# Kernel optimization log

Measured on AMD Instinct MI355X. Metric: run time of the kernel, lower is better.

The kernel has to match this reference:

```python
import jax, jax.numpy as jnp
from jax import lax
import numpy as np

NUM_Q = 3000
EMB = 256
HID = 256
B, S = 32, 500


def _gru(x, w_ih, w_hh, b_ih, b_hh):
    """PyTorch-style single-layer GRU, batch_first. x: [B,S,E] -> [B,S,H]."""
    Bn = x.shape[0]
    H = w_hh.shape[1]
    # precompute input projections for all timesteps: [B,S,3H]
    x_proj = jnp.einsum('bse,ge->bsg', x, w_ih) + b_ih

    def step(h, xp):  # h: [B,H], xp: [B,3H]
        gh = h @ w_hh.T + b_hh
        xr, xz, xn = jnp.split(xp, 3, axis=-1)
        hr, hz, hn = jnp.split(gh, 3, axis=-1)
        r = jax.nn.sigmoid(xr + hr)
        z = jax.nn.sigmoid(xz + hz)
        n = jnp.tanh(xn + r * hn)
        h_new = (1.0 - z) * n + z * h
        return h_new, h_new

    h0 = jnp.zeros((Bn, H), x.dtype)
    _, out = lax.scan(step, h0, jnp.swapaxes(x_proj, 0, 1))  # [S,B,H]
    return jnp.swapaxes(out, 0, 1)


def setup_inputs() -> dict:
    key = jax.random.key(0)
    ks = jax.random.split(key, 16)
    sc = 0.05
    inp = {
        'x': jax.random.uniform(ks[0], (B, S, 2 * NUM_Q), dtype=jnp.float32),
        'ques_h': jax.random.normal(ks[1], (2 * NUM_Q, EMB), dtype=jnp.float32) * sc,
        'ques_d': jax.random.normal(ks[2], (2 * NUM_Q, EMB), dtype=jnp.float32) * sc,
        'gru1_wih': jax.random.normal(ks[3], (3 * HID, EMB), dtype=jnp.float32) * sc,
        'gru1_whh': jax.random.normal(ks[4], (3 * HID, HID), dtype=jnp.float32) * sc,
        'gru1_bih': jnp.zeros((3 * HID,), jnp.float32),
        'gru1_bhh': jnp.zeros((3 * HID,), jnp.float32),
        'gru2_wih': jax.random.normal(ks[5], (3 * HID, EMB), dtype=jnp.float32) * sc,
        'gru2_whh': jax.random.normal(ks[6], (3 * HID, HID), dtype=jnp.float32) * sc,
        'gru2_bih': jnp.zeros((3 * HID,), jnp.float32),
        'gru2_bhh': jnp.zeros((3 * HID,), jnp.float32),
        'fcc_w': jax.random.normal(ks[7], (NUM_Q, HID), dtype=jnp.float32) * sc,
        'fcc_b': jnp.zeros((NUM_Q,), jnp.float32),
        'fct_w': jax.random.normal(ks[8], (NUM_Q, HID), dtype=jnp.float32) * sc,
        'fct_b': jnp.zeros((NUM_Q,), jnp.float32),
        'fce_w': jax.random.normal(ks[9], (NUM_Q, 2 * HID), dtype=jnp.float32) * sc,
        'fce_b': jnp.zeros((NUM_Q,), jnp.float32),
    }
    return inp


def reference(x, ques_h, ques_d,
              gru1_wih, gru1_whh, gru1_bih, gru1_bhh,
              gru2_wih, gru2_whh, gru2_bih, gru2_bhh,
              fcc_w, fcc_b, fct_w, fct_b, fce_w, fce_b):
    # interaction embeddings via question tables
    x_h = jnp.einsum('bsq,qe->bse', x, ques_h)
    x_d = jnp.einsum('bsq,qe->bse', x, ques_d)
    # dual GRU encoders
    out_h = _gru(x_h, gru1_wih, gru1_whh, gru1_bih, gru1_bhh)  # [B,S,H]
    out_d = _gru(x_d, gru2_wih, gru2_whh, gru2_bih, gru2_bhh)  # [B,S,H]
    # per-branch logits
    logit_c = jnp.einsum('bsh,qh->bsq', out_h, fcc_w) + fcc_b
    logit_t = jnp.einsum('bsh,qh->bsq', out_d, fct_w) + fct_b
    # cross-attention fusion: matmul -> softmax -> bmm, plus inverse attention
    scores = jnp.einsum('bsh,bth->bst', out_h, out_d)  # [B,S,S]
    attn = jax.nn.softmax(scores, axis=2)
    fused_d = jnp.einsum('bst,bth->bsh', attn, out_d)
    fused_h = jnp.einsum('bst,bth->bsh', 1.0 - attn, out_h)
    ens = jnp.concatenate([fused_d, fused_h], axis=-1)  # [B,S,2H]
    ensemble_logit = jnp.einsum('bsk,qk->bsq', ens, fce_w) + fce_b
    return (logit_c, logit_t, ensemble_logit)
```

## Files before the change

### kernel.cpp

```cpp
#include <hip/hip_runtime.h>
#include <math.h>

#define BATCH 32
#define SEQ   500
#define NQ    3000
#define EMB   256
#define HID   256
#define ROWS  (BATCH * SEQ)
#define X_K   (2 * NQ)

typedef short short8 __attribute__((ext_vector_type(8)));
typedef float f32x4  __attribute__((ext_vector_type(4)));

__device__ __forceinline__ unsigned bf16_rne(float f) {
    unsigned u = __float_as_uint(f);
    return (u + 0x7fffu + ((u >> 16) & 1u)) >> 16;
}
__device__ __forceinline__ unsigned pack_bf16_rn(float a, float b) {
    return bf16_rne(a) | (bf16_rne(b) << 16);
}

__device__ __forceinline__ void stage_tile(unsigned char* lbase, int row, int cg, float4 v) {
    unsigned ux = __float_as_uint(v.x), uy = __float_as_uint(v.y);
    unsigned uz = __float_as_uint(v.z), uw = __float_as_uint(v.w);
    unsigned hx = ux & 0xffff0000u, hy = uy & 0xffff0000u;
    unsigned hz = uz & 0xffff0000u, hw = uw & 0xffff0000u;
    unsigned hi01 = (hx >> 16) | hy;
    unsigned hi23 = (hz >> 16) | hw;
    unsigned lo01 = pack_bf16_rn(v.x - __uint_as_float(hx), v.y - __uint_as_float(hy));
    unsigned lo23 = pack_bf16_rn(v.z - __uint_as_float(hz), v.w - __uint_as_float(hw));
    const int slot = cg ^ (row & 7);
    const int pf   = (row >> 3) & 1;
    uint4 w = pf ? make_uint4(lo01, lo23, hi01, hi23)
                 : make_uint4(hi01, hi23, lo01, lo23);
    *reinterpret_cast<uint4*>(lbase + row * 128 + (slot << 4)) = w;
}

__device__ __forceinline__ void read_frag(const unsigned char* lbase, int row, int c,
                                          short8& hi, short8& lo) {
    const int r7 = row & 7;
    const int pf = (row >> 3) & 1;
    const unsigned char* rbase = lbase + row * 128;
    const int s0 = (((c << 1) | 0) ^ r7) << 4;
    const int s1 = (((c << 1) | 1) ^ r7) << 4;
    const int oh = pf << 3;
    const int ol = (pf ^ 1) << 3;
    uint2 h0 = *reinterpret_cast<const uint2*>(rbase + s0 + oh);
    uint2 h1 = *reinterpret_cast<const uint2*>(rbase + s1 + oh);
    uint2 l0 = *reinterpret_cast<const uint2*>(rbase + s0 + ol);
    uint2 l1 = *reinterpret_cast<const uint2*>(rbase + s1 + ol);
    hi = __builtin_bit_cast(short8, make_uint4(h0.x, h0.y, h1.x, h1.y));
    lo = __builtin_bit_cast(short8, make_uint4(l0.x, l0.y, l1.x, l1.y));
}

template<bool HASBIAS>
__global__ __launch_bounds__(256, 2)
void gemm_mfma(const float* __restrict__ A, const float* __restrict__ B,
               const float* __restrict__ bias, float* __restrict__ C,
               int M, int N, int K, int ldc,
               long long sA, long long sB, long long sC)
{
    A += (long long)blockIdx.z * sA;
    B += (long long)blockIdx.z * sB;
    C += (long long)blockIdx.z * sC;

    __shared__ __align__(16) unsigned char lds[32768];
    unsigned char* Al_ = lds;
    unsigned char* Bl_ = lds + 16384;

    const int tid = threadIdx.x;
    const int m0 = blockIdx.y * 128;
    const int n0 = blockIdx.x * 128;

    const int srow = tid >> 3;
    const int scg  = tid & 7;

    const int wid = tid >> 6;
    const int wm  = wid >> 1;
    const int wn  = wid & 1;
    const int lane = tid & 63;
    const int fr  = lane & 15;
    const int fc  = lane >> 4;

    f32x4 acc[4][4];
    #pragma unroll
    for (int i = 0; i < 4; ++i)
        #pragma unroll
        for (int j = 0; j < 4; ++j)
            acc[i][j] = (f32x4){0.f, 0.f, 0.f, 0.f};

    const int ktiles = (K + 31) >> 5;
    for (int kt = 0; kt < ktiles; ++kt) {
        const int gk = (kt << 5) + scg * 4;
        #pragma unroll
        for (int rd = 0; rd < 4; ++rd) {
            const int row = rd * 32 + srow;
            {
                const int gm = m0 + row;
                float4 v = make_float4(0.f, 0.f, 0.f, 0.f);
                if (gm < M && gk < K)
                    v = *reinterpret_cast<const float4*>(A + (long long)gm * K + gk);
                stage_tile(Al_, row, scg, v);
            }
            {
                const int gn = n0 + row;
                float4 v = make_float4(0.f, 0.f, 0.f, 0.f);
                if (gn < N && gk < K)
                    v = *reinterpret_cast<const float4*>(B + (long long)gn * K + gk);
                stage_tile(Bl_, row, scg, v);
            }
        }
        __syncthreads();

        short8 ah[4], al[4], bh[4], bl[4];
        #pragma unroll
        for (int mi = 0; mi < 4; ++mi)
            read_frag(Al_, wm * 64 + mi * 16 + fr, fc, ah[mi], al[mi]);
        #pragma unroll
        for (int ni = 0; ni < 4; ++ni)
            read_frag(Bl_, wn * 64 + ni * 16 + fr, fc, bh[ni], bl[ni]);

        #pragma unroll
        for (int mi = 0; mi < 4; ++mi) {
            #pragma unroll
            for (int ni = 0; ni < 4; ++ni) {
                acc[mi][ni] = __builtin_amdgcn_mfma_f32_16x16x32_bf16(al[mi], bh[ni], acc[mi][ni], 0, 0, 0);
                acc[mi][ni] = __builtin_amdgcn_mfma_f32_16x16x32_bf16(ah[mi], bl[ni], acc[mi][ni], 0, 0, 0);
                acc[mi][ni] = __builtin_amdgcn_mfma_f32_16x16x32_bf16(ah[mi], bh[ni], acc[mi][ni], 0, 0, 0);
            }
        }
        __syncthreads();
    }

    #pragma unroll
    for (int ni = 0; ni < 4; ++ni) {
        const int col = n0 + wn * 64 + ni * 16 + fr;
        if (col >= N) continue;
        const float bv = HASBIAS ? bias[col] : 0.f;
        #pragma unroll
        for (int mi = 0; mi < 4; ++mi) {
            #pragma unroll
            for (int q = 0; q < 4; ++q) {
                const int rw = m0 + wm * 64 + mi * 16 + fc * 4 + q;
                if (rw < M) C[(long long)rw * ldc + col] = acc[mi][ni][q] + bv;
            }
        }
    }
}

__global__ __launch_bounds__(256)
void trans_kernel(const float* __restrict__ in, float* __restrict__ out,
                  int R, int C, long long sIn, long long sOut)
{
    in  += (long long)blockIdx.z * sIn;
    out += (long long)blockIdx.z * sOut;
    __shared__ float t[32][33];
    const int r0 = blockIdx.y * 32, c0 = blockIdx.x * 32;
    const int tx = threadIdx.x & 31, ty = threadIdx.x >> 5;
    #pragma unroll
    for (int i = 0; i < 32; i += 8) {
        const int r = r0 + ty + i, c = c0 + tx;
        t[ty + i][tx] = (r < R && c < C) ? in[(long long)r * C + c] : 0.f;
    }
    __syncthreads();
    #pragma unroll
    for (int i = 0; i < 32; i += 8) {
        const int r = r0 + tx, c = c0 + ty + i;
        if (c < C && r < R) out[(long long)c * R + r] = t[tx][ty + i];
    }
}

__global__ __launch_bounds__(256)
void gru_kernel(const float* __restrict__ xp1, const float* __restrict__ xp2,
                const float* __restrict__ wT1, const float* __restrict__ wT2,
                const float* __restrict__ bh1, const float* __restrict__ bh2,
                float* __restrict__ out1, float* __restrict__ out2)
{
    const int g = blockIdx.x >> 5;
    const int b = blockIdx.x & 31;
    const float* xp = (g ? xp2 : xp1) + (long long)b * SEQ * 768;
    const float* wT = g ? wT2 : wT1;
    const float* bh = g ? bh2 : bh1;
    float* out      = (g ? out2 : out1) + (long long)b * SEQ * HID;

    __shared__ float h[HID];
    const int j = threadIdx.x;
    h[j] = 0.f;
    const float br = bh[j], bz = bh[HID + j], bn = bh[2 * HID + j];
    __syncthreads();

    for (int t = 0; t < SEQ; ++t) {
        const float* xrow = xp + (long long)t * 768;
        float ar = br, az = bz, an = bn;
        #pragma unroll 8
        for (int k = 0; k < HID; ++k) {
            const float hk = h[k];
            const float* wrow = wT + k * 768;
            ar = fmaf(hk, wrow[j], ar);
            az = fmaf(hk, wrow[HID + j], az);
            an = fmaf(hk, wrow[2 * HID + j], an);
        }
        const float r = 1.f / (1.f + __expf(-(xrow[j] + ar)));
        const float z = 1.f / (1.f + __expf(-(xrow[HID + j] + az)));
        const float n = tanhf(xrow[2 * HID + j] + r * an);
        const float hnew = (1.f - z) * n + z * h[j];
        out[(long long)t * HID + j] = hnew;
        __syncthreads();
        h[j] = hnew;
        __syncthreads();
    }
}

__global__ __launch_bounds__(256)
void softmax_kernel(float* __restrict__ s)
{
    float* p = s + (long long)blockIdx.x * SEQ;
    const int tid = threadIdx.x;
    __shared__ float red[256];

    const float v0 = (tid < SEQ) ? p[tid] : -1e30f;
    const float v1 = (tid + 256 < SEQ) ? p[tid + 256] : -1e30f;
    red[tid] = fmaxf(v0, v1);
    __syncthreads();
    for (int o = 128; o > 0; o >>= 1) {
        if (tid < o) red[tid] = fmaxf(red[tid], red[tid + o]);
        __syncthreads();
    }
    const float m = red[0];
    __syncthreads();
    const float e0 = (tid < SEQ) ? __expf(v0 - m) : 0.f;
    const float e1 = (tid + 256 < SEQ) ? __expf(v1 - m) : 0.f;
    red[tid] = e0 + e1;
    __syncthreads();
    for (int o = 128; o > 0; o >>= 1) {
        if (tid < o) red[tid] += red[tid + o];
        __syncthreads();
    }
    const float inv = 1.f / red[0];
    if (tid < SEQ) p[tid] = e0 * inv;
    if (tid + 256 < SEQ) p[tid + 256] = e1 * inv;
}

__global__ __launch_bounds__(256)
void colsum_kernel(const float* __restrict__ x, float* __restrict__ out)
{
    const int b = blockIdx.x, hh = threadIdx.x;
    const float* p = x + (long long)b * SEQ * HID + hh;
    float s = 0.f;
    for (int t = 0; t < SEQ; ++t) s += p[t * HID];
    out[b * HID + hh] = s;
}

__global__ __launch_bounds__(256)
void combine_kernel(const float* __restrict__ tmp, const float* __restrict__ cs,
                    float* __restrict__ ens)
{
    const long long r = blockIdx.x;
    const int hh = threadIdx.x;
    const int b = (int)(r / SEQ);
    ens[r * 512 + 256 + hh] = cs[b * HID + hh] - tmp[r * HID + hh];
}

extern "C" void kernel_launch(void* const* d_in, const int* in_sizes, int n_in,
                              void* d_out, int out_size, void* d_ws, size_t ws_size,
                              hipStream_t stream)
{
    const float* x      = (const float*)d_in[0];
    const float* ques_h = (const float*)d_in[1];
    const float* ques_d = (const float*)d_in[2];
    const float* w1ih   = (const float*)d_in[3];
    const float* w1hh   = (const float*)d_in[4];
    const float* b1ih   = (const float*)d_in[5];
    const float* b1hh   = (const float*)d_in[6];
    const float* w2ih   = (const float*)d_in[7];
    const float* w2hh   = (const float*)d_in[8];
    const float* b2ih   = (const float*)d_in[9];
    const float* b2hh   = (const float*)d_in[10];
    const float* fcc_w  = (const float*)d_in[11];
    const float* fcc_b  = (const float*)d_in[12];
    const float* fct_w  = (const float*)d_in[13];
    const float* fct_b  = (const float*)d_in[14];
    const float* fce_w  = (const float*)d_in[15];
    const float* fce_b  = (const float*)d_in[16];

    float* ws = (float*)d_ws;
    float* xh    = ws;
    float* xd    = ws + 4096000LL;
    float* xp1   = ws + 8192000LL;
    float* xp2   = ws + 20480000LL;
    float* outh  = ws + 32768000LL;
    float* outd  = ws + 36864000LL;
    float* wT1   = ws + 40960000LL;
    float* wT2   = ws + 41156608LL;
    float* cs    = ws + 41353216LL;
    float* quesTh = xp1;
    float* quesTd = ws + 9728000LL;
    float* attn   = xp1;
    float* ens    = xp2;
    float* tmp    = ws + 28672000LL;
    float* outhT  = ws;
    float* outdT  = ws + 4096000LL;

    float* out_c = (float*)d_out;
    float* out_t = out_c + 48000000LL;
    float* out_e = out_c + 96000000LL;

    const dim3 blk(256);

    trans_kernel<<<dim3(8, 188, 1), blk, 0, stream>>>(ques_h, quesTh, X_K, EMB, 0, 0);
    trans_kernel<<<dim3(8, 188, 1), blk, 0, stream>>>(ques_d, quesTd, X_K, EMB, 0, 0);

    gemm_mfma<false><<<dim3(2, 125, 1), blk, 0, stream>>>(
        x, quesTh, nullptr, xh, ROWS, EMB, X_K, EMB, 0, 0, 0);
    gemm_mfma<false><<<dim3(2, 125, 1), blk, 0, stream>>>(
        x, quesTd, nullptr, xd, ROWS, EMB, X_K, EMB, 0, 0, 0);

    gemm_mfma<true><<<dim3(6, 125, 1), blk, 0, stream>>>(
        xh, w1ih, b1ih, xp1, ROWS, 768, EMB, 768, 0, 0, 0);
    gemm_mfma<true><<<dim3(6, 125, 1), blk, 0, stream>>>(
        xd, w2ih, b2ih, xp2, ROWS, 768, EMB, 768, 0, 0, 0);

    trans_kernel<<<dim3(8, 24, 1), blk, 0, stream>>>(w1hh, wT1, 768, 256, 0, 0);
    trans_kernel<<<dim3(8, 24, 1), blk, 0, stream>>>(w2hh, wT2, 768, 256, 0, 0);

    gru_kernel<<<64, blk, 0, stream>>>(xp1, xp2, wT1, wT2, b1hh, b2hh, outh, outd);

    gemm_mfma<true><<<dim3(24, 125, 1), blk, 0, stream>>>(
        outh, fcc_w, fcc_b, out_c, ROWS, NQ, HID, NQ, 0, 0, 0);
    gemm_mfma<true><<<dim3(24, 125, 1), blk, 0, stream>>>(
        outd, fct_w, fct_b, out_t, ROWS, NQ, HID, NQ, 0, 0, 0);

    trans_kernel<<<dim3(8, 16, 32), blk, 0, stream>>>(outh, outhT, SEQ, HID, 128000, 128000);
    trans_kernel<<<dim3(8, 16, 32), blk, 0, stream>>>(outd, outdT, SEQ, HID, 128000, 128000);

    gemm_mfma<false><<<dim3(4, 4, 32), blk, 0, stream>>>(
        outh, outd, nullptr, attn, SEQ, SEQ, HID, SEQ,
        (long long)SEQ * HID, (long long)SEQ * HID, (long long)SEQ * SEQ);

    softmax_kernel<<<ROWS, blk, 0, stream>>>(attn);

    colsum_kernel<<<32, blk, 0, stream>>>(outh, cs);

    gemm_mfma<false><<<dim3(2, 4, 32), blk, 0, stream>>>(
        attn, outdT, nullptr, ens, SEQ, HID, SEQ, 512,
        (long long)SEQ * SEQ, (long long)HID * SEQ, (long long)SEQ * 512);
    gemm_mfma<false><<<dim3(2, 4, 32), blk, 0, stream>>>(
        attn, outhT, nullptr, tmp, SEQ, HID, SEQ, HID,
        (long long)SEQ * SEQ, (long long)HID * SEQ, (long long)SEQ * HID);

    combine_kernel<<<ROWS, blk, 0, stream>>>(tmp, cs, ens);

    gemm_mfma<true><<<dim3(24, 125, 1), blk, 0, stream>>>(
        ens, fce_w, fce_b, out_e, ROWS, NQ, 512, NQ, 0, 0, 0);
}
```

Baseline: 7.202 ms.

## Split GRU recurrence K-dimension across threads and pack two batches per block

```diff
diff --git a/kernel.cpp b/kernel.cpp
--- a/kernel.cpp
+++ b/kernel.cpp
@@ -170,43 +170,65 @@
     }
 }
 
-__global__ __launch_bounds__(256)
+__global__ __launch_bounds__(1024)
 void gru_kernel(const float* __restrict__ xp1, const float* __restrict__ xp2,
                 const float* __restrict__ wT1, const float* __restrict__ wT2,
                 const float* __restrict__ bh1, const float* __restrict__ bh2,
                 float* __restrict__ out1, float* __restrict__ out2)
 {
-    const int g = blockIdx.x >> 5;
-    const int b = blockIdx.x & 31;
+    const int g   = blockIdx.x >> 4;
+    const int bp  = blockIdx.x & 15;
+    const int tid = threadIdx.x;
+    const int j   = tid & 255;
+    const int s   = (tid >> 8) & 1;
+    const int q   = tid >> 9;
+    const int b   = bp * 2 + s;
+
     const float* xp = (g ? xp2 : xp1) + (long long)b * SEQ * 768;
     const float* wT = g ? wT2 : wT1;
     const float* bh = g ? bh2 : bh1;
     float* out      = (g ? out2 : out1) + (long long)b * SEQ * HID;
 
-    __shared__ float h[HID];
-    const int j = threadIdx.x;
-    h[j] = 0.f;
-    const float br = bh[j], bz = bh[HID + j], bn = bh[2 * HID + j];
-    __syncthreads();
+    __shared__ float h[2][HID];
+    __shared__ float pacc[2][2][3][HID];
+
+    float br = 0.f, bz = 0.f, bn = 0.f;
+    if (tid < 512) {
+        h[s][j] = 0.f;
+        br = bh[j]; bz = bh[HID + j]; bn = bh[2 * HID + j];
+    }
+    __syncthreads();
+
+    const float* wbase = wT + (long long)q * 128 * 768;
+    const float* hrow  = &h[s][q * 128];
 
     for (int t = 0; t < SEQ; ++t) {
-        const float* xrow = xp + (long long)t * 768;
-        float ar = br, az = bz, an = bn;
+        float ar = 0.f, az = 0.f, an = 0.f;
         #pragma unroll 8
-        for (int k = 0; k < HID; ++k) {
-            const float hk = h[k];
-            const float* wrow = wT + k * 768;
+        for (int k = 0; k < 128; ++k) {
+            const float hk = hrow[k];
+            const float* wrow = wbase + k * 768;
             ar = fmaf(hk, wrow[j], ar);
             az = fmaf(hk, wrow[HID + j], az);
             an = fmaf(hk, wrow[2 * HID + j], an);
         }
-        const float r = 1.f / (1.f + __expf(-(xrow[j] + ar)));
-        const float z = 1.f / (1.f + __expf(-(xrow[HID + j] + az)));
-        const float n = tanhf(xrow[2 * HID + j] + r * an);
-        const float hnew = (1.f - z) * n + z * h[j];
-        out[(long long)t * HID + j] = hnew;
-        __syncthreads();
-        h[j] = hnew;
+        pacc[s][q][0][j] = ar;
+        pacc[s][q][1][j] = az;
+        pacc[s][q][2][j] = an;
+        __syncthreads();
+
+        if (tid < 512) {
+            const float* xrow = xp + (long long)t * 768;
+            const float gr = pacc[s][0][0][j] + pacc[s][1][0][j] + br;
+            const float gz = pacc[s][0][1][j] + pacc[s][1][1][j] + bz;
+            const float gn = pacc[s][0][2][j] + pacc[s][1][2][j] + bn;
+            const float r = 1.f / (1.f + __expf(-(xrow[j] + gr)));
+            const float z = 1.f / (1.f + __expf(-(xrow[HID + j] + gz)));
+            const float n = tanhf(xrow[2 * HID + j] + r * gn);
+            const float hnew = (1.f - z) * n + z * h[s][j];
+            out[(long long)t * HID + j] = hnew;
+            h[s][j] = hnew;
+        }
         __syncthreads();
     }
 }
@@ -323,7 +345,7 @@
     trans_kernel<<<dim3(8, 24, 1), blk, 0, stream>>>(w1hh, wT1, 768, 256, 0, 0);
     trans_kernel<<<dim3(8, 24, 1), blk, 0, stream>>>(w2hh, wT2, 768, 256, 0, 0);
 
-    gru_kernel<<<64, blk, 0, stream>>>(xp1, xp2, wT1, wT2, b1hh, b2hh, outh, outd);
+    gru_kernel<<<32, dim3(1024), 0, stream>>>(xp1, xp2, wT1, wT2, b1hh, b2hh, outh, outd);
 
     gemm_mfma<true><<<dim3(24, 125, 1), blk, 0, stream>>>(
         outh, fcc_w, fcc_b, out_c, ROWS, NQ, HID, NQ, 0, 0, 0);
```

Measured after the change: 9.166 ms. +27.3%, slower.

## Split GRU recurrence across four cooperating blocks with register-resident weights

Applied to the files above, without the earlier changes.

```diff
diff --git a/kernel.cpp b/kernel.cpp
--- a/kernel.cpp
+++ b/kernel.cpp
@@ -171,43 +171,124 @@
 }
 
 __global__ __launch_bounds__(256)
+void gru_init_kernel(float* __restrict__ h_g, unsigned* __restrict__ pflag,
+                     unsigned* __restrict__ hflag)
+{
+    const int i = blockIdx.x * 256 + threadIdx.x;
+    if (i < 64 * HID) h_g[i] = 0.f;
+    if (i < 64) { pflag[i] = 0u; hflag[i] = 0u; }
+}
+
+__global__ __launch_bounds__(256, 1)
 void gru_kernel(const float* __restrict__ xp1, const float* __restrict__ xp2,
                 const float* __restrict__ wT1, const float* __restrict__ wT2,
                 const float* __restrict__ bh1, const float* __restrict__ bh2,
-                float* __restrict__ out1, float* __restrict__ out2)
-{
-    const int g = blockIdx.x >> 5;
-    const int b = blockIdx.x & 31;
-    const float* xp = (g ? xp2 : xp1) + (long long)b * SEQ * 768;
+                float* __restrict__ out1, float* __restrict__ out2,
+                float* __restrict__ partials, float* __restrict__ h_g,
+                unsigned* __restrict__ pflag, unsigned* __restrict__ hflag)
+{
+    __shared__ float h_lds[HID];
+
+    const int bid = blockIdx.x;
+    const int grp = bid >> 2;
+    const int kq  = bid & 3;
+    const int g   = grp >> 5;
+    const int b   = grp & 31;
+    const int tid = threadIdx.x;
+    const int j   = tid;
+
     const float* wT = g ? wT2 : wT1;
-    const float* bh = g ? bh2 : bh1;
-    float* out      = (g ? out2 : out1) + (long long)b * SEQ * HID;
-
-    __shared__ float h[HID];
-    const int j = threadIdx.x;
-    h[j] = 0.f;
-    const float br = bh[j], bz = bh[HID + j], bn = bh[2 * HID + j];
-    __syncthreads();
-
-    for (int t = 0; t < SEQ; ++t) {
-        const float* xrow = xp + (long long)t * 768;
-        float ar = br, az = bz, an = bn;
-        #pragma unroll 8
-        for (int k = 0; k < HID; ++k) {
-            const float hk = h[k];
-            const float* wrow = wT + k * 768;
-            ar = fmaf(hk, wrow[j], ar);
-            az = fmaf(hk, wrow[HID + j], az);
-            an = fmaf(hk, wrow[2 * HID + j], an);
-        }
-        const float r = 1.f / (1.f + __expf(-(xrow[j] + ar)));
-        const float z = 1.f / (1.f + __expf(-(xrow[HID + j] + az)));
-        const float n = tanhf(xrow[2 * HID + j] + r * an);
-        const float hnew = (1.f - z) * n + z * h[j];
-        out[(long long)t * HID + j] = hnew;
+    float* part     = partials + ((long long)grp * 4 + kq) * 768;
+    float* hg       = h_g + grp * HID;
+    unsigned* pf    = pflag + grp;
+    unsigned* hf    = hflag + grp;
+
+    float wreg[64][3];
+    {
+        const float* wb = wT + (long long)(64 * kq) * 768 + j;
+        #pragma unroll
+        for (int kl = 0; kl < 64; ++kl) {
+            wreg[kl][0] = wb[kl * 768];
+            wreg[kl][1] = wb[kl * 768 + 256];
+            wreg[kl][2] = wb[kl * 768 + 512];
+        }
+    }
+
+    if (kq == 0) {
+        const float* xp = (g ? xp2 : xp1) + (long long)b * SEQ * 768;
+        const float* bh = g ? bh2 : bh1;
+        float* out      = (g ? out2 : out1) + (long long)b * SEQ * HID;
+        const float br = bh[j], bz = bh[HID + j], bn = bh[2 * HID + j];
+
+        h_lds[j] = 0.f;
         __syncthreads();
-        h[j] = hnew;
-        __syncthreads();
+
+        for (int t = 0; t < SEQ; ++t) {
+            const float* xrow = xp + (long long)t * 768;
+            const float xr = xrow[j], xz = xrow[HID + j], xn = xrow[2 * HID + j];
+
+            float ar = 0.f, az = 0.f, an = 0.f;
+            #pragma unroll
+            for (int kl = 0; kl < 64; ++kl) {
+                const float hk = h_lds[kl];
+                ar = fmaf(wreg[kl][0], hk, ar);
+                az = fmaf(wreg[kl][1], hk, az);
+                an = fmaf(wreg[kl][2], hk, an);
+            }
+
+            if (tid == 0) {
+                const unsigned target = 3u * (unsigned)(t + 1);
+                while (__hip_atomic_load(pf, __ATOMIC_ACQUIRE, __HIP_MEMORY_SCOPE_AGENT) < target)
+                    __builtin_amdgcn_s_sleep(2);
+            }
+            __syncthreads();
+
+            float gr = ar + br, gz = az + bz, gn = an + bn;
+            #pragma unroll
+            for (int q2 = 1; q2 < 4; ++q2) {
+                const float* pp = partials + ((long long)grp * 4 + q2) * 768;
+                gr += __hip_atomic_load(&pp[j],           __ATOMIC_RELAXED, __HIP_MEMORY_SCOPE_AGENT);
+                gz += __hip_atomic_load(&pp[HID + j],     __ATOMIC_RELAXED, __HIP_MEMORY_SCOPE_AGENT);
+                gn += __hip_atomic_load(&pp[2 * HID + j], __ATOMIC_RELAXED, __HIP_MEMORY_SCOPE_AGENT);
+            }
+            const float r = 1.f / (1.f + __expf(-(xr + gr)));
+            const float z = 1.f / (1.f + __expf(-(xz + gz)));
+            const float n = tanhf(xn + r * gn);
+            const float hnew = (1.f - z) * n + z * h_lds[j];
+            out[(long long)t * HID + j] = hnew;
+            __hip_atomic_store(&hg[j], hnew, __ATOMIC_RELAXED, __HIP_MEMORY_SCOPE_AGENT);
+            h_lds[j] = hnew;
+            __syncthreads();
+            if (tid == 0)
+                __hip_atomic_fetch_add(hf, 1u, __ATOMIC_RELEASE, __HIP_MEMORY_SCOPE_AGENT);
+        }
+    } else {
+        for (int t = 0; t < SEQ; ++t) {
+            if (tid == 0) {
+                while (__hip_atomic_load(hf, __ATOMIC_ACQUIRE, __HIP_MEMORY_SCOPE_AGENT) < (unsigned)t)
+                    __builtin_amdgcn_s_sleep(2);
+            }
+            __syncthreads();
+            if (tid < 64)
+                h_lds[tid] = __hip_atomic_load(&hg[64 * kq + tid],
+                                               __ATOMIC_RELAXED, __HIP_MEMORY_SCOPE_AGENT);
+            __syncthreads();
+
+            float ar = 0.f, az = 0.f, an = 0.f;
+            #pragma unroll
+            for (int kl = 0; kl < 64; ++kl) {
+                const float hk = h_lds[kl];
+                ar = fmaf(wreg[kl][0], hk, ar);
+                az = fmaf(wreg[kl][1], hk, az);
+                an = fmaf(wreg[kl][2], hk, an);
+            }
+            __hip_atomic_store(&part[j],           ar, __ATOMIC_RELAXED, __HIP_MEMORY_SCOPE_AGENT);
+            __hip_atomic_store(&part[HID + j],     az, __ATOMIC_RELAXED, __HIP_MEMORY_SCOPE_AGENT);
+            __hip_atomic_store(&part[2 * HID + j], an, __ATOMIC_RELAXED, __HIP_MEMORY_SCOPE_AGENT);
+            __syncthreads();
+            if (tid == 0)
+                __hip_atomic_fetch_add(pf, 1u, __ATOMIC_RELEASE, __HIP_MEMORY_SCOPE_AGENT);
+        }
     }
 }
 
@@ -300,6 +381,10 @@
     float* tmp    = ws + 28672000LL;
     float* outhT  = ws;
     float* outdT  = ws + 4096000LL;
+    float*    gpart = ws;
+    float*    ghg   = ws + 196608LL;
+    unsigned* gpf   = (unsigned*)(ws + 212992LL);
+    unsigned* ghf   = (unsigned*)(ws + 213056LL);
 
     float* out_c = (float*)d_out;
     float* out_t = out_c + 48000000LL;
@@ -323,7 +408,9 @@
     trans_kernel<<<dim3(8, 24, 1), blk, 0, stream>>>(w1hh, wT1, 768, 256, 0, 0);
     trans_kernel<<<dim3(8, 24, 1), blk, 0, stream>>>(w2hh, wT2, 768, 256, 0, 0);
 
-    gru_kernel<<<64, blk, 0, stream>>>(xp1, xp2, wT1, wT2, b1hh, b2hh, outh, outd);
+    gru_init_kernel<<<64, blk, 0, stream>>>(ghg, gpf, ghf);
+    gru_kernel<<<256, blk, 0, stream>>>(xp1, xp2, wT1, wT2, b1hh, b2hh, outh, outd,
+                                        gpart, ghg, gpf, ghf);
 
     gemm_mfma<true><<<dim3(24, 125, 1), blk, 0, stream>>>(
         outh, fcc_w, fcc_b, out_c, ROWS, NQ, HID, NQ, 0, 0, 0);
```

After: 11.31 ms. +57.1%, slower.

## Pre-pack GEMM operands into split-bf16 layout before MFMA kernels

Applied to the files above, without the earlier changes.

```diff
diff --git a/kernel.cpp b/kernel.cpp
--- a/kernel.cpp
+++ b/kernel.cpp
@@ -19,8 +19,7 @@
 __device__ __forceinline__ unsigned pack_bf16_rn(float a, float b) {
     return bf16_rne(a) | (bf16_rne(b) << 16);
 }
-
-__device__ __forceinline__ void stage_tile(unsigned char* lbase, int row, int cg, float4 v) {
+__device__ __forceinline__ uint4 pack_group(float4 v, int pf) {
     unsigned ux = __float_as_uint(v.x), uy = __float_as_uint(v.y);
     unsigned uz = __float_as_uint(v.z), uw = __float_as_uint(v.w);
     unsigned hx = ux & 0xffff0000u, hy = uy & 0xffff0000u;
@@ -29,11 +28,16 @@
     unsigned hi23 = (hz >> 16) | hw;
     unsigned lo01 = pack_bf16_rn(v.x - __uint_as_float(hx), v.y - __uint_as_float(hy));
     unsigned lo23 = pack_bf16_rn(v.z - __uint_as_float(hz), v.w - __uint_as_float(hw));
-    const int slot = cg ^ (row & 7);
-    const int pf   = (row >> 3) & 1;
-    uint4 w = pf ? make_uint4(lo01, lo23, hi01, hi23)
-                 : make_uint4(hi01, hi23, lo01, lo23);
-    *reinterpret_cast<uint4*>(lbase + row * 128 + (slot << 4)) = w;
+    return pf ? make_uint4(lo01, lo23, hi01, hi23)
+              : make_uint4(hi01, hi23, lo01, lo23);
+}
+
+__device__ __forceinline__ void stage_f32(unsigned char* lbase, int row, int cg, float4 v) {
+    *reinterpret_cast<uint4*>(lbase + row * 128 + (((cg ^ (row & 7))) << 4)) =
+        pack_group(v, (row >> 3) & 1);
+}
+__device__ __forceinline__ void stage_pk(unsigned char* lbase, int row, int cg, uint4 w) {
+    *reinterpret_cast<uint4*>(lbase + row * 128 + (((cg ^ (row & 7))) << 4)) = w;
 }
 
 __device__ __forceinline__ void read_frag(const unsigned char* lbase, int row, int c,
@@ -53,16 +57,33 @@
     lo = __builtin_bit_cast(short8, make_uint4(l0.x, l0.y, l1.x, l1.y));
 }
 
-template<bool HASBIAS>
+__global__ __launch_bounds__(256)
+void convert_kernel(const float* __restrict__ in, uint4* __restrict__ out,
+                    long long ngroups, int rg, int rpb)
+{
+    long long i = (long long)blockIdx.x * 256 + threadIdx.x;
+    const long long stride = (long long)gridDim.x * 256;
+    for (; i < ngroups; i += stride) {
+        float4 v = *reinterpret_cast<const float4*>(in + i * 4);
+        const int row = (int)((i / rg) % rpb);
+        out[i] = pack_group(v, (row >> 3) & 1);
+    }
+}
+
+template<bool HASBIAS, bool CONVA>
 __global__ __launch_bounds__(256, 2)
-void gemm_mfma(const float* __restrict__ A, const float* __restrict__ B,
+void gemm_mfma(const void* Av, const uint4* __restrict__ Bpk,
                const float* __restrict__ bias, float* __restrict__ C,
                int M, int N, int K, int ldc,
                long long sA, long long sB, long long sC)
 {
-    A += (long long)blockIdx.z * sA;
-    B += (long long)blockIdx.z * sB;
-    C += (long long)blockIdx.z * sC;
+    const float* Af  = (const float*)Av;
+    const uint4* Apk = (const uint4*)Av;
+    if (CONVA) Af  += (long long)blockIdx.z * sA;
+    else       Apk += (long long)blockIdx.z * sA;
+    Bpk += (long long)blockIdx.z * sB;
+    C   += (long long)blockIdx.z * sC;
+    const int Kg = K >> 2;
 
     __shared__ __align__(16) unsigned char lds[32768];
     unsigned char* Al_ = lds;
@@ -97,17 +118,24 @@
             const int row = rd * 32 + srow;
             {
                 const int gm = m0 + row;
-                float4 v = make_float4(0.f, 0.f, 0.f, 0.f);
-                if (gm < M && gk < K)
-                    v = *reinterpret_cast<const float4*>(A + (long long)gm * K + gk);
-                stage_tile(Al_, row, scg, v);
+                if (CONVA) {
+                    float4 v = make_float4(0.f, 0.f, 0.f, 0.f);
+                    if (gm < M && gk < K)
+                        v = *reinterpret_cast<const float4*>(Af + (long long)gm * K + gk);
+                    stage_f32(Al_, row, scg, v);
+                } else {
+                    uint4 w = make_uint4(0u, 0u, 0u, 0u);
+                    if (gm < M && gk < K)
+                        w = Apk[(long long)gm * Kg + (gk >> 2)];
+                    stage_pk(Al_, row, scg, w);
+                }
             }
             {
                 const int gn = n0 + row;
-                float4 v = make_float4(0.f, 0.f, 0.f, 0.f);
+                uint4 w = make_uint4(0u, 0u, 0u, 0u);
                 if (gn < N && gk < K)
-                    v = *reinterpret_cast<const float4*>(B + (long long)gn * K + gk);
-                stage_tile(Bl_, row, scg, v);
+                    w = Bpk[(long long)gn * Kg + (gk >> 2)];
+                stage_pk(Bl_, row, scg, w);
             }
         }
         __syncthreads();
@@ -293,63 +321,87 @@
     float* wT1   = ws + 40960000LL;
     float* wT2   = ws + 41156608LL;
     float* cs    = ws + 41353216LL;
-    float* quesTh = xp1;
-    float* quesTd = ws + 9728000LL;
-    float* attn   = xp1;
-    float* ens    = xp2;
-    float* tmp    = ws + 28672000LL;
-    float* outhT  = ws;
-    float* outdT  = ws + 4096000LL;
+    uint4* fcc_c = (uint4*)(ws + 41361408LL);
+    uint4* fct_c = (uint4*)(ws + 42129408LL);
+    uint4* fce_c = (uint4*)(ws + 42897408LL);
+    uint4* w1c   = (uint4*)(ws + 44433408LL);
+    uint4* w2c   = (uint4*)(ws + 44630016LL);
+    float* qT1   = ws + 8192000LL;
+    float* qT2   = ws + 9728000LL;
+    float* attn  = ws + 8192000LL;
+    float* ens   = ws + 20480000LL;
+    float* tmp   = ws + 28672000LL;
+    float* outhT = ws;
+    float* outdT = ws + 4096000LL;
+    uint4* oh_apk = (uint4*)(ws + 20480000LL);
+    uint4* od_apk = (uint4*)(ws + 24576000LL);
 
     float* out_c = (float*)d_out;
     float* out_t = out_c + 48000000LL;
     float* out_e = out_c + 96000000LL;
 
     const dim3 blk(256);
-
-    trans_kernel<<<dim3(8, 188, 1), blk, 0, stream>>>(ques_h, quesTh, X_K, EMB, 0, 0);
-    trans_kernel<<<dim3(8, 188, 1), blk, 0, stream>>>(ques_d, quesTd, X_K, EMB, 0, 0);
-
-    gemm_mfma<false><<<dim3(2, 125, 1), blk, 0, stream>>>(
-        x, quesTh, nullptr, xh, ROWS, EMB, X_K, EMB, 0, 0, 0);
-    gemm_mfma<false><<<dim3(2, 125, 1), blk, 0, stream>>>(
-        x, quesTd, nullptr, xd, ROWS, EMB, X_K, EMB, 0, 0, 0);
-
-    gemm_mfma<true><<<dim3(6, 125, 1), blk, 0, stream>>>(
-        xh, w1ih, b1ih, xp1, ROWS, 768, EMB, 768, 0, 0, 0);
-    gemm_mfma<true><<<dim3(6, 125, 1), blk, 0, stream>>>(
-        xd, w2ih, b2ih, xp2, ROWS, 768, EMB, 768, 0, 0, 0);
+    const dim3 cgrid(1024);
+
+    trans_kernel<<<dim3(8, 188, 1), blk, 0, stream>>>(ques_h, qT1, X_K, EMB, 0, 0);
+    trans_kernel<<<dim3(8, 188, 1), blk, 0, stream>>>(ques_d, qT2, X_K, EMB, 0, 0);
+    convert_kernel<<<cgrid, blk, 0, stream>>>(qT1, (uint4*)qT1, 384000, 1500, 256);
+    convert_kernel<<<cgrid, blk, 0, stream>>>(qT2, (uint4*)qT2, 384000, 1500, 256);
+    convert_kernel<<<cgrid, blk, 0, stream>>>(w1ih, w1c, 49152, 64, 768);
+    convert_kernel<<<cgrid, blk, 0, stream>>>(w2ih, w2c, 49152, 64, 768);
+    convert_kernel<<<cgrid, blk, 0, stream>>>(fcc_w, fcc_c, 192000, 64, 3000);
+    convert_kernel<<<cgrid, blk, 0, stream>>>(fct_w, fct_c, 192000, 64, 3000);
+    convert_kernel<<<cgrid, blk, 0, stream>>>(fce_w, fce_c, 384000, 128, 3000);
+
+    gemm_mfma<false, true><<<dim3(2, 125, 1), blk, 0, stream>>>(
+        x, (uint4*)qT1, nullptr, xh, ROWS, EMB, X_K, EMB, 0, 0, 0);
+    gemm_mfma<false, true><<<dim3(2, 125, 1), blk, 0, stream>>>(
+        x, (uint4*)qT2, nullptr, xd, ROWS, EMB, X_K, EMB, 0, 0, 0);
+
+    convert_kernel<<<cgrid, blk, 0, stream>>>(xh, (uint4*)xh, 1024000, 64, ROWS);
+    convert_kernel<<<cgrid, blk, 0, stream>>>(xd, (uint4*)xd, 1024000, 64, ROWS);
+    gemm_mfma<true, false><<<dim3(6, 125, 1), blk, 0, stream>>>(
+        (uint4*)xh, w1c, b1ih, xp1, ROWS, 768, EMB, 768, 0, 0, 0);
+    gemm_mfma<true, false><<<dim3(6, 125, 1), blk, 0, stream>>>(
+        (uint4*)xd, w2c, b2ih, xp2, ROWS, 768, EMB, 768, 0, 0, 0);
 
     trans_kernel<<<dim3(8, 24, 1), blk, 0, stream>>>(w1hh, wT1, 768, 256, 0, 0);
     trans_kernel<<<dim3(8, 24, 1), blk, 0, stream>>>(w2hh, wT2, 768, 256, 0, 0);
 
     gru_kernel<<<64, blk, 0, stream>>>(xp1, xp2, wT1, wT2, b1hh, b2hh, outh, outd);
 
-    gemm_mfma<true><<<dim3(24, 125, 1), blk, 0, stream>>>(
-        outh, fcc_w, fcc_b, out_c, ROWS, NQ, HID, NQ, 0, 0, 0);
-    gemm_mfma<true><<<dim3(24, 125, 1), blk, 0, stream>>>(
-        outd, fct_w, fct_b, out_t, ROWS, NQ, HID, NQ, 0, 0, 0);
-
     trans_kernel<<<dim3(8, 16, 32), blk, 0, stream>>>(outh, outhT, SEQ, HID, 128000, 128000);
     trans_kernel<<<dim3(8, 16, 32), blk, 0, stream>>>(outd, outdT, SEQ, HID, 128000, 128000);
-
-    gemm_mfma<false><<<dim3(4, 4, 32), blk, 0, stream>>>(
-        outh, outd, nullptr, attn, SEQ, SEQ, HID, SEQ,
-        (long long)SEQ * HID, (long long)SEQ * HID, (long long)SEQ * SEQ);
+    colsum_kernel<<<32, blk, 0, stream>>>(outh, cs);
+
+    convert_kernel<<<cgrid, blk, 0, stream>>>(outh, oh_apk, 1024000, 64, SEQ);
+    convert_kernel<<<cgrid, blk, 0, stream>>>(outd, od_apk, 1024000, 64, SEQ);
+    convert_kernel<<<cgrid, blk, 0, stream>>>(outh, (uint4*)outh, 1024000, 64, ROWS);
+    convert_kernel<<<cgrid, blk, 0, stream>>>(outd, (uint4*)outd, 1024000, 64, ROWS);
+    convert_kernel<<<cgrid, blk, 0, stream>>>(outhT, (uint4*)outhT, 1024000, 125, 256);
+    convert_kernel<<<cgrid, blk, 0, stream>>>(outdT, (uint4*)outdT, 1024000, 125, 256);
+
+    gemm_mfma<true, false><<<dim3(24, 125, 1), blk, 0, stream>>>(
+        (uint4*)outh, fcc_c, fcc_b, out_c, ROWS, NQ, HID, NQ, 0, 0, 0);
+    gemm_mfma<true, false><<<dim3(24, 125, 1), blk, 0, stream>>>(
+        (uint4*)outd, fct_c, fct_b, out_t, ROWS, NQ, HID, NQ, 0, 0, 0);
+
+    gemm_mfma<false, false><<<dim3(4, 4, 32), blk, 0, stream>>>(
+        oh_apk, od_apk, nullptr, attn, SEQ, SEQ, HID, SEQ,
+        32000, 32000, (long long)SEQ * SEQ);
 
     softmax_kernel<<<ROWS, blk, 0, stream>>>(attn);
-
-    colsum_kernel<<<32, blk, 0, stream>>>(outh, cs);
-
-    gemm_mfma<false><<<dim3(2, 4, 32), blk, 0, stream>>>(
-        attn, outdT, nullptr, ens, SEQ, HID, SEQ, 512,
-        (long long)SEQ * SEQ, (long long)HID * SEQ, (long long)SEQ * 512);
-    gemm_mfma<false><<<dim3(2, 4, 32), blk, 0, stream>>>(
-        attn, outhT, nullptr, tmp, SEQ, HID, SEQ, HID,
-        (long long)SEQ * SEQ, (long long)HID * SEQ, (long long)SEQ * HID);
+    convert_kernel<<<cgrid, blk, 0, stream>>>(attn, (uint4*)attn, 2000000, 125, SEQ);
+
+    gemm_mfma<false, false><<<dim3(2, 4, 32), blk, 0, stream>>>(
+        (uint4*)attn, (uint4*)outdT, nullptr, ens, SEQ, HID, SEQ, 512,
+        62500, 32000, (long long)SEQ * 512);
+    gemm_mfma<false, false><<<dim3(2, 4, 32), blk, 0, stream>>>(
+        (uint4*)attn, (uint4*)outhT, nullptr, tmp, SEQ, HID, SEQ, HID,
+        62500, 32000, (long long)SEQ * HID);
 
     combine_kernel<<<ROWS, blk, 0, stream>>>(tmp, cs, ens);
-
-    gemm_mfma<true><<<dim3(24, 125, 1), blk, 0, stream>>>(
-        ens, fce_w, fce_b, out_e, ROWS, NQ, 512, NQ, 0, 0, 0);
-}
+    convert_kernel<<<cgrid, blk, 0, stream>>>(ens, (uint4*)ens, 2048000, 128, ROWS);
+    gemm_mfma<true, false><<<dim3(24, 125, 1), blk, 0, stream>>>(
+        (uint4*)ens, fce_c, fce_b, out_e, ROWS, NQ, 512, NQ, 0, 0, 0);
+}
```

Measured after the change: 7.144 ms. No clear change (-0.8%).
